# Optimization experiments

Measured on AMD Instinct MI355X. Metric: run time of the kernel, lower is better.

The kernel has to match this reference:

```python
import jax, jax.numpy as jnp
import numpy as np

PAST = 12
FUTURE = 12
INPUT_SIZE = 256
OUTPUT_SIZE = FUTURE * INPUT_SIZE  # 3072


def setup_inputs() -> dict:
    key = jax.random.key(0)
    k_inp, k_w, k_b = jax.random.split(key, 3)
    inp = jax.random.normal(k_inp, (64, 288, INPUT_SIZE), dtype=jnp.float32)
    fan_in = INPUT_SIZE * PAST
    bound = 1.0 / np.sqrt(fan_in)
    # torch nn.Linear init: U(-1/sqrt(fan_in), 1/sqrt(fan_in)); W is (out, in)
    W = jax.random.uniform(k_w, (OUTPUT_SIZE, fan_in), minval=-bound, maxval=bound, dtype=jnp.float32)
    b = jax.random.uniform(k_b, (OUTPUT_SIZE,), minval=-bound, maxval=bound, dtype=jnp.float32)
    return {"inp": inp, "W": W, "b": b}


def reference(inp, W, b):
    batch, length, dim = inp.shape
    n_win = length - PAST  # number of sliding windows (torch loop count)
    # Gather all overlapping windows at once: (batch, n_win, PAST, dim)
    idx = jnp.arange(n_win)[:, None] + jnp.arange(PAST)[None, :]
    windows = inp[:, idx, :].reshape(batch, n_win, PAST * dim)
    # One batched GEMM replaces n_win tiny Linear calls: x @ W.T + b
    out = jnp.einsum('bnk,ok->bno', windows, W) + b
    return out.reshape(batch, -1, FUTURE, dim)
```

## Files before the change

### kernel.cpp

```cpp
#include <hip/hip_runtime.h>
#include <hip/hip_bf16.h>

#define BATCH   64
#define LEN     288
#define DIM     256
#define PAST    12
#define NWIN    (LEN - PAST)
#define M_DIM   (BATCH * NWIN)
#define K_DIM   (PAST * DIM)
#define N_DIM   3072

#define BM 256
#define BN 256
#define BK 64
#define NTILE   (K_DIM / BK)
#define NITER   (NTILE / 2)

#define GRID_N   12
#define BULK_WG  768
#define TAIL_M0  16384
#define TAIL_QN  24
#define TAIL_WG  240

typedef __attribute__((ext_vector_type(8))) short bh8;
typedef __attribute__((ext_vector_type(4))) float f32x4;

__device__ __forceinline__ void llds16(const void* g, void* l) {
    __builtin_amdgcn_global_load_lds(
        (const __attribute__((address_space(1))) unsigned int*)g,
        (__attribute__((address_space(3))) unsigned int*)l,
        16, 0, 0);
}

__global__ void cvt_f32_bf16(const float* __restrict__ in,
                             __hip_bfloat16* __restrict__ out, int n8) {
    int i = blockIdx.x * blockDim.x + threadIdx.x;
    if (i >= n8) return;
    const float4* p = (const float4*)in;
    float4 a = p[2 * i], b = p[2 * i + 1];
    union { __hip_bfloat16 h[8]; int4 v; } u;
    u.h[0] = __float2bfloat16(a.x); u.h[1] = __float2bfloat16(a.y);
    u.h[2] = __float2bfloat16(a.z); u.h[3] = __float2bfloat16(a.w);
    u.h[4] = __float2bfloat16(b.x); u.h[5] = __float2bfloat16(b.y);
    u.h[6] = __float2bfloat16(b.z); u.h[7] = __float2bfloat16(b.w);
    ((int4*)out)[i] = u.v;
}

#define PH_MID  __builtin_amdgcn_sched_barrier(0); __builtin_amdgcn_s_barrier(); \
                __builtin_amdgcn_sched_barrier(0); __builtin_amdgcn_s_setprio(1);
#define PH_END  __builtin_amdgcn_s_setprio(0); __builtin_amdgcn_sched_barrier(0); \
                __builtin_amdgcn_s_barrier(); __builtin_amdgcn_sched_barrier(0);
#define PH_END_VM(N) __builtin_amdgcn_s_setprio(0); __builtin_amdgcn_sched_barrier(0); \
                asm volatile("s_waitcnt vmcnt(" #N ")" ::: "memory"); \
                __builtin_amdgcn_s_barrier(); __builtin_amdgcn_sched_barrier(0);

#define LDS_A(buf) (smem + (buf) * 65536)
#define LDS_B(buf) (smem + (buf) * 65536 + 32768)

#define RD_AK(buf, MB, KO, dst) { \
    const char* _b = LDS_A(buf) + aRowB; \
    _Pragma("unroll") for (int mi = 0; mi < 4; ++mi) \
        dst[mi] = *(const bh8*)(_b + ((MB) + mi) * 2048 + (KO)); }
#define RD_BK(buf, KO, dst) { \
    const char* _b = LDS_B(buf) + bRowB; \
    _Pragma("unroll") for (int ni = 0; ni < 4; ++ni) \
        dst[ni] = *(const bh8*)(_b + ni * 2048 + (KO)); }
#define MFMA_K(MB, AS, BS) \
    _Pragma("unroll") for (int mi = 0; mi < 4; ++mi) \
    _Pragma("unroll") for (int ni = 0; ni < 4; ++ni) \
        acc[(MB) + mi][ni] = __builtin_amdgcn_mfma_f32_16x16x32_bf16( \
            AS[mi], BS[ni], acc[(MB) + mi][ni], 0, 0, 0);
#define STG_A1(buf, kt, q) \
    llds16(Ag + aSrc[q] + (kt) * 64, LDS_A(buf) + (q) * 8192 + wOff);
#define STG_B1(buf, kt, u) \
    llds16(Wg + bSrc[u] + (kt) * 64, LDS_B(buf) + (u) * 8192 + wOff);

__global__ __launch_bounds__(512, 2)
void gemm_bulk(const __hip_bfloat16* __restrict__ Ag,
               const __hip_bfloat16* __restrict__ Wg,
               const float* __restrict__ bias,
               float* __restrict__ C)
{
    extern __shared__ char smem[];

    const int tid = threadIdx.x;
    const int wgid = (blockIdx.x & 7) * (BULK_WG / 8) + (blockIdx.x >> 3);
    const int bm = wgid / GRID_N;
    const int bn = wgid - bm * GRID_N;
    const int tile_m = bm * BM;
    const int tile_n = bn * BN;

    const int rd  = tid >> 3;
    const int chs = (((tid & 7) ^ (rd & 7)) * 8);
    int aSrc[4], bSrc[4];
#pragma unroll
    for (int rb = 0; rb < 4; ++rb) {
        int m  = tile_m + rb * 64 + rd;
        int bq = m / NWIN;
        int wq = m - bq * NWIN;
        aSrc[rb] = (bq * LEN + wq) * DIM + chs;
        bSrc[rb] = (tile_n + rb * 64 + rd) * K_DIM + chs;
    }

    const int wave = tid >> 6, lane = tid & 63;
    const int wm = wave >> 2, wn = wave & 3;
    const int fr = lane & 15, kg = lane >> 4;
    const int sw    = (fr & 7) << 4;
    const int kOff0 = (kg * 16) ^ sw;
    const int kOff1 = kOff0 ^ 64;
    const int aRowB = (wm * 128 + fr) * 128;
    const int bRowB = (wn * 64 + fr) * 128;
    const int wOff  = wave * 1024;

    bh8 aP[4], aQ[4], bP[4], bQ[4];
    f32x4 acc[8][4] = {};

    STG_A1(0, 0, 0); STG_A1(0, 0, 1); STG_A1(0, 0, 2); STG_A1(0, 0, 3);
    STG_B1(0, 0, 0); STG_B1(0, 0, 1); STG_B1(0, 0, 2); STG_B1(0, 0, 3);
    STG_A1(1, 1, 0); STG_A1(1, 1, 2);
    STG_B1(1, 1, 0); STG_B1(1, 1, 1);
    STG_A1(1, 1, 1); STG_A1(1, 1, 3);
    asm volatile("s_waitcnt vmcnt(6)" ::: "memory");
    __builtin_amdgcn_s_barrier();
    __builtin_amdgcn_sched_barrier(0);

    RD_AK(0, 0, kOff0, aP); RD_BK(0, kOff0, bP);

#pragma unroll 1
    for (int it = 0; it < NITER; ++it) {
        const int b = 2 * it + 1;
        int c = 2 * it + 2; if (c >= NTILE) c = NTILE - 2;
        int d = 2 * it + 3; if (d >= NTILE) d = NTILE - 1;

        RD_AK(0, 0, kOff1, aQ); RD_BK(0, kOff1, bQ);
        STG_B1(1, b, 2); STG_B1(1, b, 3);
        PH_MID; MFMA_K(0, aP, bP); PH_END;

        RD_AK(0, 4, kOff0, aP);
        STG_A1(0, c, 0); STG_A1(0, c, 2);
        PH_MID; MFMA_K(0, aQ, bQ); PH_END;

        RD_AK(0, 4, kOff1, aQ);
        STG_B1(0, c, 0); STG_B1(0, c, 1);
        PH_MID; MFMA_K(4, aP, bP); PH_END_VM(4);

        RD_AK(1, 0, kOff0, aP); RD_BK(1, kOff0, bP);
        STG_A1(0, c, 1); STG_A1(0, c, 3);
        PH_MID; MFMA_K(4, aQ, bQ); PH_END;

        RD_AK(1, 0, kOff1, aQ); RD_BK(1, kOff1, bQ);
        STG_B1(0, c, 2); STG_B1(0, c, 3);
        PH_MID; MFMA_K(0, aP, bP); PH_END;

        RD_AK(1, 4, kOff0, aP);
        STG_A1(1, d, 0); STG_A1(1, d, 2);
        PH_MID; MFMA_K(0, aQ, bQ); PH_END;

        RD_AK(1, 4, kOff1, aQ);
        STG_B1(1, d, 0); STG_B1(1, d, 1);
        PH_MID; MFMA_K(4, aP, bP); PH_END_VM(4);

        RD_AK(0, 0, kOff0, aP); RD_BK(0, kOff0, bP);
        STG_A1(1, d, 1); STG_A1(1, d, 3);
        PH_MID; MFMA_K(4, aQ, bQ); PH_END;
    }

    float bv[4];
    const float* bp = bias + tile_n + wn * 64 + fr;
#pragma unroll
    for (int ni = 0; ni < 4; ++ni) bv[ni] = bp[ni * 16];

    const int r0 = (lane >> 4) * 4;
#pragma unroll
    for (int mi = 0; mi < 8; ++mi) {
#pragma unroll
        for (int j = 0; j < 4; ++j) {
            long m = tile_m + wm * 128 + mi * 16 + r0 + j;
            float* crow = C + m * (long)N_DIM + tile_n + wn * 64 + fr;
#pragma unroll
            for (int ni = 0; ni < 4; ++ni)
                __builtin_nontemporal_store(acc[mi][ni][j] + bv[ni], &crow[ni * 16]);
        }
    }
}

#define TLDS_A(buf) (smem + (buf) * 32768)
#define TLDS_B(buf) (smem + (buf) * 32768 + 16384)

#define T_RD(buf) { \
    const char* _bb = TLDS_B(buf) + bRowB; \
    _Pragma("unroll") for (int ni = 0; ni < 2; ++ni) { \
        fb0[ni][0] = *(const bh8*)(_bb + ni * 2048 + kOff0); \
        fb0[ni][1] = *(const bh8*)(_bb + ni * 2048 + kOff1); \
    } \
    const char* _a = TLDS_A(buf) + aRowB; \
    _Pragma("unroll") for (int mi = 0; mi < 4; ++mi) { \
        a0[mi][0] = *(const bh8*)(_a + mi * 2048 + kOff0); \
        a0[mi][1] = *(const bh8*)(_a + mi * 2048 + kOff1); \
    } }
#define T_MFMA(MB) \
    _Pragma("unroll") for (int mi = 0; mi < 2; ++mi) \
    _Pragma("unroll") for (int ni = 0; ni < 2; ++ni) { \
        acc[MB + mi][ni] = __builtin_amdgcn_mfma_f32_16x16x32_bf16( \
            a0[MB + mi][0], fb0[ni][0], acc[MB + mi][ni], 0, 0, 0); \
        acc[MB + mi][ni] = __builtin_amdgcn_mfma_f32_16x16x32_bf16( \
            a0[MB + mi][1], fb0[ni][1], acc[MB + mi][ni], 0, 0, 0); \
    }
#define T_STG_A(buf, kt, u) \
    llds16(Ag + aSrc[u] + (kt) * 64, TLDS_A(buf) + (u) * 8192 + wOff);
#define T_STG_B(buf, kt, u) \
    llds16(Wg + bSrc[u] + (kt) * 64, TLDS_B(buf) + (u) * 8192 + wOff);

__global__ __launch_bounds__(512, 2)
void gemm_tail(const __hip_bfloat16* __restrict__ Ag,
               const __hip_bfloat16* __restrict__ Wg,
               const float* __restrict__ bias,
               float* __restrict__ C)
{
    extern __shared__ char smem[];

    const int tid = threadIdx.x;
    const int wgid = (blockIdx.x & 7) * (TAIL_WG / 8) + (blockIdx.x >> 3);
    const int qm = wgid / TAIL_QN;
    const int qn = wgid - qm * TAIL_QN;
    const int tile_m = TAIL_M0 + qm * 128;
    const int tile_n = qn * 128;

    const int rd  = tid >> 3;
    const int chs = (((tid & 7) ^ (rd & 7)) * 8);
    int aSrc[2], bSrc[2];
#pragma unroll
    for (int rb = 0; rb < 2; ++rb) {
        int m  = tile_m + rb * 64 + rd;
        int bq = m / NWIN;
        int wq = m - bq * NWIN;
        aSrc[rb] = (bq * LEN + wq) * DIM + chs;
        bSrc[rb] = (tile_n + rb * 64 + rd) * K_DIM + chs;
    }

    const int wave = tid >> 6, lane = tid & 63;
    const int wm = wave >> 2, wn = wave & 3;
    const int fr = lane & 15, kg = lane >> 4;
    const int sw    = (fr & 7) << 4;
    const int kOff0 = (kg * 16) ^ sw;
    const int kOff1 = kOff0 ^ 64;
    const int aRowB = (wm * 64 + fr) * 128;
    const int bRowB = (wn * 32 + fr) * 128;
    const int wOff  = wave * 1024;

    bh8 a0[4][2], fb0[2][2];
    f32x4 acc[4][2] = {};

    T_STG_A(0, 0, 0); T_STG_A(0, 0, 1); T_STG_B(0, 0, 0); T_STG_B(0, 0, 1);
    T_STG_A(1, 1, 0); T_STG_A(1, 1, 1);
    asm volatile("s_waitcnt vmcnt(2)" ::: "memory");
    __builtin_amdgcn_s_barrier();
    __builtin_amdgcn_sched_barrier(0);

#pragma unroll 1
    for (int it = 0; it < NITER; ++it) {
        const int b = 2 * it + 1;
        int c = 2 * it + 2; if (c >= NTILE) c = NTILE - 2;
        int d = 2 * it + 3; if (d >= NTILE) d = NTILE - 1;

        T_RD(0);
        T_STG_B(1, b, 0); T_STG_B(1, b, 1);
        PH_MID; T_MFMA(0); PH_END;

        T_STG_A(0, c, 0); T_STG_A(0, c, 1);
        PH_MID; T_MFMA(2); PH_END_VM(2);

        T_RD(1);
        T_STG_B(0, c, 0); T_STG_B(0, c, 1);
        PH_MID; T_MFMA(0); PH_END;

        T_STG_A(1, d, 0); T_STG_A(1, d, 1);
        PH_MID; T_MFMA(2); PH_END_VM(2);
    }

    float bv[2];
    const float* bp = bias + tile_n + wn * 32 + fr;
#pragma unroll
    for (int ni = 0; ni < 2; ++ni) bv[ni] = bp[ni * 16];

    const int r0 = (lane >> 4) * 4;
#pragma unroll
    for (int mi = 0; mi < 4; ++mi) {
#pragma unroll
        for (int j = 0; j < 4; ++j) {
            long m = tile_m + wm * 64 + mi * 16 + r0 + j;
            float* crow = C + m * (long)N_DIM + tile_n + wn * 32 + fr;
#pragma unroll
            for (int ni = 0; ni < 2; ++ni)
                __builtin_nontemporal_store(acc[mi][ni][j] + bv[ni], &crow[ni * 16]);
        }
    }
}

extern "C" void kernel_launch(void* const* d_in, const int* in_sizes, int n_in,
                              void* d_out, int out_size, void* d_ws, size_t ws_size,
                              hipStream_t stream) {
    const float* inp  = (const float*)d_in[0];
    const float* Wf   = (const float*)d_in[1];
    const float* bias = (const float*)d_in[2];
    float* out = (float*)d_out;

    __hip_bfloat16* Abf = (__hip_bfloat16*)d_ws;
    __hip_bfloat16* Wbf = (__hip_bfloat16*)((char*)d_ws + (size_t)BATCH * LEN * DIM * 2);

    const int nA8 = BATCH * LEN * DIM / 8;
    const int nW8 = N_DIM * K_DIM / 8;
    cvt_f32_bf16<<<(nA8 + 255) / 256, 256, 0, stream>>>(inp, Abf, nA8);
    cvt_f32_bf16<<<(nW8 + 255) / 256, 256, 0, stream>>>(Wf, Wbf, nW8);

    hipFuncSetAttribute((const void*)gemm_bulk,
                        hipFuncAttributeMaxDynamicSharedMemorySize, 131072);
    hipFuncSetAttribute((const void*)gemm_tail,
                        hipFuncAttributeMaxDynamicSharedMemorySize, 65536);
    gemm_bulk<<<dim3(BULK_WG), 512, 131072, stream>>>(Abf, Wbf, bias, out);
    gemm_tail<<<dim3(TAIL_WG), 512, 65536, stream>>>(Abf, Wbf, bias, out);
}
```

Baseline: 308.1 us.

## Load A operand directly from global into registers, stage only W in LDS

The bulk GEMM stops staging the activation (A) tile through LDS. Each wave now loads its A fragments straight from global memory into registers using precomputed per-row window offsets, and only the weight tile is double-buffered in LDS. This halves LDS use to 64 KB per workgroup and removes the LDS write/read traffic for A. The cost is that A rows shared across waves (the wn dimension) are fetched redundantly from global/L2, and the loads are smaller and less coalesced. Several sched_barrier fences were also removed, which gives the compiler more freedom to reorder around the barriers.

```diff
diff --git a/kernel.cpp b/kernel.cpp
--- a/kernel.cpp
+++ b/kernel.cpp
@@ -46,34 +46,29 @@
     ((int4*)out)[i] = u.v;
 }
 
-#define PH_MID  __builtin_amdgcn_sched_barrier(0); __builtin_amdgcn_s_barrier(); \
-                __builtin_amdgcn_sched_barrier(0); __builtin_amdgcn_s_setprio(1);
-#define PH_END  __builtin_amdgcn_s_setprio(0); __builtin_amdgcn_sched_barrier(0); \
-                __builtin_amdgcn_s_barrier(); __builtin_amdgcn_sched_barrier(0);
-#define PH_END_VM(N) __builtin_amdgcn_s_setprio(0); __builtin_amdgcn_sched_barrier(0); \
+#define PH_MID  __builtin_amdgcn_s_barrier(); __builtin_amdgcn_s_setprio(1);
+#define PH_END  __builtin_amdgcn_s_setprio(0); __builtin_amdgcn_s_barrier();
+#define PH_END_VM(N) __builtin_amdgcn_s_setprio(0); \
                 asm volatile("s_waitcnt vmcnt(" #N ")" ::: "memory"); \
-                __builtin_amdgcn_s_barrier(); __builtin_amdgcn_sched_barrier(0);
-
-#define LDS_A(buf) (smem + (buf) * 65536)
-#define LDS_B(buf) (smem + (buf) * 65536 + 32768)
-
-#define RD_AK(buf, MB, KO, dst) { \
-    const char* _b = LDS_A(buf) + aRowB; \
-    _Pragma("unroll") for (int mi = 0; mi < 4; ++mi) \
-        dst[mi] = *(const bh8*)(_b + ((MB) + mi) * 2048 + (KO)); }
-#define RD_BK(buf, KO, dst) { \
-    const char* _b = LDS_B(buf) + bRowB; \
+                __builtin_amdgcn_s_barrier();
+
+#define BLDS(buf) (smem + (buf) * 32768)
+
+#define RD_B4(buf, dst, KO) { \
+    const char* _b = BLDS(buf) + bRowB; \
     _Pragma("unroll") for (int ni = 0; ni < 4; ++ni) \
         dst[ni] = *(const bh8*)(_b + ni * 2048 + (KO)); }
-#define MFMA_K(MB, AS, BS) \
+#define GA4(dst, mi0, ktv, half) { \
+    _Pragma("unroll") for (int mi = 0; mi < 4; ++mi) \
+        dst[mi] = *(const bh8*)((const char*)Ag + \
+            (size_t)(unsigned)(aoffB[(mi0) + mi] + (ktv) * 128 + (half) * 64)); }
+#define MFMA_K16(MB, AS, BS) \
     _Pragma("unroll") for (int mi = 0; mi < 4; ++mi) \
     _Pragma("unroll") for (int ni = 0; ni < 4; ++ni) \
         acc[(MB) + mi][ni] = __builtin_amdgcn_mfma_f32_16x16x32_bf16( \
             AS[mi], BS[ni], acc[(MB) + mi][ni], 0, 0, 0);
-#define STG_A1(buf, kt, q) \
-    llds16(Ag + aSrc[q] + (kt) * 64, LDS_A(buf) + (q) * 8192 + wOff);
-#define STG_B1(buf, kt, u) \
-    llds16(Wg + bSrc[u] + (kt) * 64, LDS_B(buf) + (u) * 8192 + wOff);
+#define BSTG(buf, kt, u) \
+    llds16(Wg + bSrc[u] + (kt) * 64, BLDS(buf) + (u) * 8192 + wOff);
 
 __global__ __launch_bounds__(512, 2)
 void gemm_bulk(const __hip_bfloat16* __restrict__ Ag,
@@ -92,15 +87,10 @@
 
     const int rd  = tid >> 3;
     const int chs = (((tid & 7) ^ (rd & 7)) * 8);
-    int aSrc[4], bSrc[4];
-#pragma unroll
-    for (int rb = 0; rb < 4; ++rb) {
-        int m  = tile_m + rb * 64 + rd;
-        int bq = m / NWIN;
-        int wq = m - bq * NWIN;
-        aSrc[rb] = (bq * LEN + wq) * DIM + chs;
+    int bSrc[4];
+#pragma unroll
+    for (int rb = 0; rb < 4; ++rb)
         bSrc[rb] = (tile_n + rb * 64 + rd) * K_DIM + chs;
-    }
 
     const int wave = tid >> 6, lane = tid & 63;
     const int wm = wave >> 2, wn = wave & 3;
@@ -108,61 +98,63 @@
     const int sw    = (fr & 7) << 4;
     const int kOff0 = (kg * 16) ^ sw;
     const int kOff1 = kOff0 ^ 64;
-    const int aRowB = (wm * 128 + fr) * 128;
     const int bRowB = (wn * 64 + fr) * 128;
     const int wOff  = wave * 1024;
 
-    bh8 aP[4], aQ[4], bP[4], bQ[4];
+    int aoffB[8];
+#pragma unroll
+    for (int mi = 0; mi < 8; ++mi) {
+        int m  = tile_m + wm * 128 + mi * 16 + fr;
+        int bq = m / NWIN;
+        int wq = m - bq * NWIN;
+        aoffB[mi] = ((bq * LEN + wq) * DIM + kg * 8) * 2;
+    }
+
+    bh8 aP[4], aQ[4], bK0[4], bK1[4];
     f32x4 acc[8][4] = {};
 
-    STG_A1(0, 0, 0); STG_A1(0, 0, 1); STG_A1(0, 0, 2); STG_A1(0, 0, 3);
-    STG_B1(0, 0, 0); STG_B1(0, 0, 1); STG_B1(0, 0, 2); STG_B1(0, 0, 3);
-    STG_A1(1, 1, 0); STG_A1(1, 1, 2);
-    STG_B1(1, 1, 0); STG_B1(1, 1, 1);
-    STG_A1(1, 1, 1); STG_A1(1, 1, 3);
-    asm volatile("s_waitcnt vmcnt(6)" ::: "memory");
+    BSTG(0, 0, 0); BSTG(0, 0, 1); BSTG(0, 0, 2); BSTG(0, 0, 3);
+    BSTG(1, 1, 0); BSTG(1, 1, 1); BSTG(1, 1, 2); BSTG(1, 1, 3);
+    GA4(aP, 0, 0, 0);
+    asm volatile("s_waitcnt vmcnt(8)" ::: "memory");
     __builtin_amdgcn_s_barrier();
-    __builtin_amdgcn_sched_barrier(0);
-
-    RD_AK(0, 0, kOff0, aP); RD_BK(0, kOff0, bP);
 
 #pragma unroll 1
     for (int it = 0; it < NITER; ++it) {
-        const int b = 2 * it + 1;
-        int c = 2 * it + 2; if (c >= NTILE) c = NTILE - 2;
-        int d = 2 * it + 3; if (d >= NTILE) d = NTILE - 1;
-
-        RD_AK(0, 0, kOff1, aQ); RD_BK(0, kOff1, bQ);
-        STG_B1(1, b, 2); STG_B1(1, b, 3);
-        PH_MID; MFMA_K(0, aP, bP); PH_END;
-
-        RD_AK(0, 4, kOff0, aP);
-        STG_A1(0, c, 0); STG_A1(0, c, 2);
-        PH_MID; MFMA_K(0, aQ, bQ); PH_END;
-
-        RD_AK(0, 4, kOff1, aQ);
-        STG_B1(0, c, 0); STG_B1(0, c, 1);
-        PH_MID; MFMA_K(4, aP, bP); PH_END_VM(4);
-
-        RD_AK(1, 0, kOff0, aP); RD_BK(1, kOff0, bP);
-        STG_A1(0, c, 1); STG_A1(0, c, 3);
-        PH_MID; MFMA_K(4, aQ, bQ); PH_END;
-
-        RD_AK(1, 0, kOff1, aQ); RD_BK(1, kOff1, bQ);
-        STG_B1(0, c, 2); STG_B1(0, c, 3);
-        PH_MID; MFMA_K(0, aP, bP); PH_END;
-
-        RD_AK(1, 4, kOff0, aP);
-        STG_A1(1, d, 0); STG_A1(1, d, 2);
-        PH_MID; MFMA_K(0, aQ, bQ); PH_END;
-
-        RD_AK(1, 4, kOff1, aQ);
-        STG_B1(1, d, 0); STG_B1(1, d, 1);
-        PH_MID; MFMA_K(4, aP, bP); PH_END_VM(4);
-
-        RD_AK(0, 0, kOff0, aP); RD_BK(0, kOff0, bP);
-        STG_A1(1, d, 1); STG_A1(1, d, 3);
-        PH_MID; MFMA_K(4, aQ, bQ); PH_END;
+        const int kt0 = 2 * it, kt1 = 2 * it + 1;
+        const int t2  = (it < NITER - 1) ? 2 * it + 2 : NTILE - 2;
+        const int t3  = (it < NITER - 1) ? 2 * it + 3 : NTILE - 1;
+        const int tn0 = (it < NITER - 1) ? 2 * it + 2 : 0;
+
+        RD_B4(0, bK0, kOff0);
+        GA4(aQ, 0, kt0, 1);
+        PH_MID; MFMA_K16(0, aP, bK0); PH_END;
+
+        RD_B4(0, bK1, kOff1);
+        GA4(aP, 4, kt0, 0);
+        PH_MID; MFMA_K16(0, aQ, bK1); PH_END;
+
+        GA4(aQ, 4, kt0, 1);
+        BSTG(0, t2, 0); BSTG(0, t2, 1); BSTG(0, t2, 2); BSTG(0, t2, 3);
+        PH_MID; MFMA_K16(4, aP, bK0); PH_END;
+
+        GA4(aP, 0, kt1, 0);
+        PH_MID; MFMA_K16(4, aQ, bK1); PH_END_VM(4);
+
+        RD_B4(1, bK0, kOff0);
+        GA4(aQ, 0, kt1, 1);
+        PH_MID; MFMA_K16(0, aP, bK0); PH_END;
+
+        RD_B4(1, bK1, kOff1);
+        GA4(aP, 4, kt1, 0);
+        PH_MID; MFMA_K16(0, aQ, bK1); PH_END;
+
+        GA4(aQ, 4, kt1, 1);
+        BSTG(1, t3, 0); BSTG(1, t3, 1); BSTG(1, t3, 2); BSTG(1, t3, 3);
+        PH_MID; MFMA_K16(4, aP, bK0); PH_END;
+
+        GA4(aP, 0, tn0, 0);
+        PH_MID; MFMA_K16(4, aQ, bK1); PH_END_VM(4);
     }
 
     float bv[4];
@@ -255,7 +247,6 @@
     T_STG_A(1, 1, 0); T_STG_A(1, 1, 1);
     asm volatile("s_waitcnt vmcnt(2)" ::: "memory");
     __builtin_amdgcn_s_barrier();
-    __builtin_amdgcn_sched_barrier(0);
 
 #pragma unroll 1
     for (int it = 0; it < NITER; ++it) {
@@ -314,9 +305,9 @@
     cvt_f32_bf16<<<(nW8 + 255) / 256, 256, 0, stream>>>(Wf, Wbf, nW8);
 
     hipFuncSetAttribute((const void*)gemm_bulk,
-                        hipFuncAttributeMaxDynamicSharedMemorySize, 131072);
+                        hipFuncAttributeMaxDynamicSharedMemorySize, 65536);
     hipFuncSetAttribute((const void*)gemm_tail,
                         hipFuncAttributeMaxDynamicSharedMemorySize, 65536);
-    gemm_bulk<<<dim3(BULK_WG), 512, 131072, stream>>>(Abf, Wbf, bias, out);
+    gemm_bulk<<<dim3(BULK_WG), 512, 65536, stream>>>(Abf, Wbf, bias, out);
     gemm_tail<<<dim3(TAIL_WG), 512, 65536, stream>>>(Abf, Wbf, bias, out);
 }
```

Result: slower. 687.1 us (+123.1%).
